# Kernel tuning notes

Measured on AMD Instinct MI355X. Metric: run time of the kernel, lower is better.

The kernel has to match this reference:

```python
import jax, jax.numpy as jnp
import numpy as np

N_ATOM_BASIS = 128
MAX_Z = 100
N_GAUSSIANS = 25
N_FILTERS = 128
R_CUTOFF = 5.0


def ssp(x):
    # shifted softplus: log(0.5*exp(x) + 0.5)
    return jax.nn.softplus(x) - jnp.log(2.0).astype(x.dtype)


def setup_inputs() -> dict:
    key = jax.random.key(0)
    ks = jax.random.split(key, 12)
    N, K = 20000, 48
    dR = jax.random.uniform(ks[0], (N, K), jnp.float32) * R_CUTOFF
    Z = jax.random.randint(ks[1], (N,), 0, MAX_Z, jnp.int32)
    neighbor_idx = jax.random.randint(ks[2], (N, K), 0, N + 1, jnp.int32)  # idx == N is padding
    s = 1.0 / np.sqrt(N_ATOM_BASIS)
    return {
        "dR": dR,
        "Z": Z,
        "neighbor_idx": neighbor_idx,
        "embed": jax.random.normal(ks[3], (MAX_Z, N_ATOM_BASIS), jnp.float32),
        "in2f_w": jax.random.normal(ks[4], (N_ATOM_BASIS, N_FILTERS), jnp.float32) * s,
        "f1_w": jax.random.normal(ks[5], (N_GAUSSIANS, N_FILTERS), jnp.float32) * (1.0 / np.sqrt(N_GAUSSIANS)),
        "f1_b": jnp.zeros((N_FILTERS,), jnp.float32),
        "f2_w": jax.random.normal(ks[6], (N_FILTERS, N_FILTERS), jnp.float32) * s,
        "f2_b": jnp.zeros((N_FILTERS,), jnp.float32),
        "o1_w": jax.random.normal(ks[7], (N_FILTERS, N_ATOM_BASIS), jnp.float32) * s,
        "o1_b": jnp.zeros((N_ATOM_BASIS,), jnp.float32),
        "o2_w": jax.random.normal(ks[8], (N_ATOM_BASIS, N_ATOM_BASIS), jnp.float32) * s,
        "o2_b": jnp.zeros((N_ATOM_BASIS,), jnp.float32),
    }


def reference(dR, Z, neighbor_idx, embed, in2f_w, f1_w, f1_b, f2_w, f2_b,
              o1_w, o1_b, o2_w, o2_b):
    N = Z.shape[0]
    # atom embedding [N, 128]
    x = embed[Z]

    # gaussian smearing of distances [N, K, 25]
    offsets = jnp.linspace(0.0, R_CUTOFF, N_GAUSSIANS, dtype=jnp.float32)
    width = offsets[1] - offsets[0]
    coeff = -0.5 / (width * width)
    g = jnp.exp(coeff * jnp.square(dR[..., None] - offsets))

    # filter-generating network [N, K, F]
    W = ssp(g @ f1_w + f1_b) @ f2_w + f2_b

    # cosine cutoff and pairwise (padding) mask
    cut = 0.5 * (jnp.cos(dR * (jnp.pi / R_CUTOFF)) + 1.0) * (dR < R_CUTOFF)
    mask = (neighbor_idx < N).astype(jnp.float32)  # [N, K]
    W = W * (cut * mask)[..., None]

    # continuous-filter convolution: project, gather neighbors, weight, aggregate
    y = x @ in2f_w                                  # [N, F]
    idx_safe = jnp.where(neighbor_idx < N, neighbor_idx, 0)
    y_nb = y[idx_safe]                              # [N, K, F] gather
    agg = jnp.sum(y_nb * W, axis=1)                 # [N, F]

    # output network + residual
    v = ssp(agg @ o1_w + o1_b) @ o2_w + o2_b
    return x + v
```

## Files before the change

kernel.cpp:

```cpp
#include <hip/hip_runtime.h>
#include <hip/hip_fp16.h>
#include <math.h>

constexpr int F    = 128;
constexpr int KN   = 48;
constexpr int NG   = 25;
constexpr int TN   = 176;
constexpr int MAXZ = 100;

typedef _Float16 f16x8 __attribute__((ext_vector_type(8)));
typedef float    f32x4 __attribute__((ext_vector_type(4)));

__device__ __forceinline__ float ssp(float x) {
    return fmaxf(x, 0.0f) + __logf(fmaf(0.5f, __expf(-fabsf(x)), 0.5f));
}

__device__ __forceinline__ unsigned short f2h(float x) {
    return __half_as_ushort(__float2half_rn(x));
}
__device__ __forceinline__ __half2 u2h2(unsigned int u) {
    union { unsigned int u; __half2 h; } c; c.u = u; return c.h;
}

__global__ __launch_bounds__(256) void k_prep(
    const float* __restrict__ f1w, const float* __restrict__ f1b,
    const float* __restrict__ f2w, const float* __restrict__ f2b,
    const float* __restrict__ o1w, const float* __restrict__ o2w,
    const float* __restrict__ embed, const float* __restrict__ in2f,
    unsigned int* __restrict__ tabp, unsigned int* __restrict__ yzp,
    unsigned short* __restrict__ o1f, unsigned short* __restrict__ o2f, int N)
{
    __shared__ float s0[F];
    __shared__ float s1[F];
    int bid = blockIdx.x;
    int tid = threadIdx.x;

    if (bid < TN + 1) {
        int j = bid, f = tid;
        float d = (float)j * (5.0f / (float)TN);
        constexpr float width = 5.0f / 24.0f;
        constexpr float coeff = -0.5f / (width * width);
        if (f < F) {
            float z = f1b[f];
            #pragma unroll
            for (int c = 0; c < NG; ++c) {
                float t = d - (float)c * width;
                z = fmaf(__expf(coeff * t * t), f1w[c * F + f], z);
            }
            s0[f] = ssp(z);
        }
        __syncthreads();
        if (f < F) {
            float w = f2b[f];
            #pragma unroll 8
            for (int c = 0; c < F; ++c)
                w = fmaf(s0[c], f2w[c * F + f], w);
            float cut = 0.5f * (cosf(d * 0.62831853071795864769f) + 1.0f);
            cut = (d < 5.0f) ? cut : 0.0f;
            s1[f] = w * cut;
        }
        __syncthreads();
        if (f < 64)
            tabp[j * 64 + f] = (unsigned int)f2h(s1[2 * f]) | ((unsigned int)f2h(s1[2 * f + 1]) << 16);
        return;
    }
    bid -= TN + 1;

    if (bid < 128) {
        int t = bid * 256 + tid;
        int e = t & 16383;
        int j = e & 7, l = (e >> 3) & 63, nt = (e >> 9) & 7, kt = e >> 12;
        int k = kt * 32 + ((l >> 4) << 3) + j;
        int col = nt * 16 + (l & 15);
        if (t < 16384) o1f[e] = f2h(o1w[k * F + col]);
        else           o2f[e] = f2h(o2w[k * F + col]);
        return;
    }
    bid -= 128;

    {
        int z = bid, f = tid;
        if (z < MAXZ) {
            if (f < F) s0[f] = embed[z * F + f];
            __syncthreads();
            if (f < F) {
                float acc = 0.f;
                #pragma unroll 8
                for (int c = 0; c < F; ++c)
                    acc = fmaf(s0[c], in2f[c * F + f], acc);
                s1[f] = acc;
            }
        } else {
            if (f < F) s1[f] = 0.f;
            __syncthreads();
        }
        __syncthreads();
        if (f < 64)
            yzp[z * 64 + f] = (unsigned int)f2h(s1[2 * f]) | ((unsigned int)f2h(s1[2 * f + 1]) << 16);
    }
}

__global__ __launch_bounds__(512, 6) void k_main(
    const float* __restrict__ dR, const int* __restrict__ nbr,
    const int* __restrict__ Z,
    const unsigned int* __restrict__ tabp,
    const unsigned int* __restrict__ yzp,
    const unsigned short* __restrict__ o1f, const float* __restrict__ o1b,
    const unsigned short* __restrict__ o2f, const float* __restrict__ o2b,
    const float* __restrict__ embed,
    float* __restrict__ out, int N, int ngroups)
{
    extern __shared__ unsigned int smem[];
    unsigned int*   tabL = smem;
    unsigned int*   aggL = smem + 11328;
    unsigned short* Us   = (unsigned short*)(smem + 11328 + 1024);

    int tid  = threadIdx.x;
    int wid  = tid >> 6;
    int lane = tid & 63;
    int lr   = lane & 15;
    int lg   = lane >> 4;

    for (int m = tid; m < (TN + 1) * 64; m += 512)
        tabL[m] = tabp[m];
    __syncthreads();

    for (int g = blockIdx.x; g < ngroups; g += gridDim.x) {
        int n0 = g * 16;

        int aA = wid * 2, aB = aA + 1;
        int nA = n0 + aA, nB = n0 + aB;
        float a0 = 0.f, a1 = 0.f, b0 = 0.f, b1 = 0.f;
        if (nA < N) {
            int mB = (nB < N) ? nB : nA;

            unsigned int pA = 0, pB = 0;
            if (lane < KN) {
                float dA = dR[nA * KN + lane];
                int   iA = nbr[nA * KN + lane];
                float uA = dA * ((float)TN / 5.0f);
                int   jA = (int)uA; jA = (jA > TN - 1) ? (TN - 1) : jA;
                float fA = uA - (float)jA;
                unsigned int zA = (iA >= 0 && iA < N) ? (unsigned int)Z[iA] : (unsigned int)MAXZ;
                pA = ((unsigned int)f2h(fA) << 16) | ((unsigned int)jA << 7) | zA;

                float dB = dR[mB * KN + lane];
                int   iB = nbr[mB * KN + lane];
                float uB = dB * ((float)TN / 5.0f);
                int   jB = (int)uB; jB = (jB > TN - 1) ? (TN - 1) : jB;
                float fB = uB - (float)jB;
                unsigned int zB = (iB >= 0 && iB < N) ? (unsigned int)Z[iB] : (unsigned int)MAXZ;
                pB = ((unsigned int)f2h(fB) << 16) | ((unsigned int)jB << 7) | zB;
            }

            #pragma unroll
            for (int c = 0; c < 4; ++c) {
                __half2 pacA = u2h2(0u);
                __half2 pacB = u2h2(0u);
                #pragma unroll
                for (int k2 = 0; k2 < 12; ++k2) {
                    int k = c * 12 + k2;
                    unsigned int qA = (unsigned int)__builtin_amdgcn_readlane((int)pA, k);
                    unsigned int qB = (unsigned int)__builtin_amdgcn_readlane((int)pB, k);

                    __half2 frA = u2h2((qA & 0xFFFF0000u) | (qA >> 16));
                    __half2 frB = u2h2((qB & 0xFFFF0000u) | (qB >> 16));
                    unsigned int jbA = (qA & 0x7F80u) << 1;
                    unsigned int jbB = (qB & 0x7F80u) << 1;
                    unsigned int zbA = (qA & 0x7Fu) << 8;
                    unsigned int zbB = (qB & 0x7Fu) << 8;

                    const unsigned int* rA = (const unsigned int*)((const char*)tabL + jbA);
                    const unsigned int* rB = (const unsigned int*)((const char*)tabL + jbB);
                    __half2 tA0 = u2h2(rA[lane]);
                    __half2 tA1 = u2h2(rA[lane + 64]);
                    __half2 tB0 = u2h2(rB[lane]);
                    __half2 tB1 = u2h2(rB[lane + 64]);
                    __half2 yA  = u2h2(*(const unsigned int*)((const char*)yzp + zbA + (lane << 2)));
                    __half2 yB  = u2h2(*(const unsigned int*)((const char*)yzp + zbB + (lane << 2)));

                    __half2 wA = __hfma2(frA, __hsub2(tA1, tA0), tA0);
                    __half2 wB = __hfma2(frB, __hsub2(tB1, tB0), tB0);
                    pacA = __hfma2(wA, yA, pacA);
                    pacB = __hfma2(wB, yB, pacB);
                }
                float2 fa = __half22float2(pacA); a0 += fa.x; a1 += fa.y;
                float2 fb = __half22float2(pacB); b0 += fb.x; b1 += fb.y;
            }
        }
        aggL[aA * 64 + (lane ^ (aA << 2))] = (unsigned int)f2h(a0) | ((unsigned int)f2h(a1) << 16);
        aggL[aB * 64 + (lane ^ (aB << 2))] = (unsigned int)f2h(b0) | ((unsigned int)f2h(b1) << 16);
        __syncthreads();

        f32x4 c1 = {0.f, 0.f, 0.f, 0.f};
        #pragma unroll
        for (int kt = 0; kt < 4; ++kt) {
            f16x8 b = *reinterpret_cast<const f16x8*>(o1f + (((kt * 8 + wid) * 64 + lane) << 3));
            const char* ap = (const char*)aggL + lr * 256 + ((kt * 64 + lg * 16) ^ (lr << 4));
            f16x8 a = *reinterpret_cast<const f16x8*>(ap);
            c1 = __builtin_amdgcn_mfma_f32_16x16x32_f16(a, b, c1, 0, 0, 0);
        }
        int fcol = wid * 16 + lr;
        float bv1 = o1b[fcol];
        #pragma unroll
        for (int jr = 0; jr < 4; ++jr) {
            int r = lg * 4 + jr;
            float u = ssp(c1[jr] + bv1);
            Us[r * F + (fcol ^ (r << 3))] = f2h(u);
        }
        __syncthreads();

        f32x4 c2 = {0.f, 0.f, 0.f, 0.f};
        #pragma unroll
        for (int kt = 0; kt < 4; ++kt) {
            f16x8 b = *reinterpret_cast<const f16x8*>(o2f + (((kt * 8 + wid) * 64 + lane) << 3));
            f16x8 a = *reinterpret_cast<const f16x8*>(&Us[lr * F + ((kt * 32 + lg * 8) ^ (lr << 3))]);
            c2 = __builtin_amdgcn_mfma_f32_16x16x32_f16(a, b, c2, 0, 0, 0);
        }
        float bv2 = o2b[fcol];
        #pragma unroll
        for (int jr = 0; jr < 4; ++jr) {
            int r = lg * 4 + jr;
            int n = n0 + r;
            if (n < N) {
                float x = embed[Z[n] * F + fcol];
                out[n * F + fcol] = x + c2[jr] + bv2;
            }
        }
    }
}

extern "C" void kernel_launch(void* const* d_in, const int* in_sizes, int n_in,
                              void* d_out, int out_size, void* d_ws, size_t ws_size,
                              hipStream_t stream) {
    const float* dR    = (const float*)d_in[0];
    const int*   Z     = (const int*)  d_in[1];
    const int*   nbr   = (const int*)  d_in[2];
    const float* embed = (const float*)d_in[3];
    const float* in2f  = (const float*)d_in[4];
    const float* f1w   = (const float*)d_in[5];
    const float* f1b   = (const float*)d_in[6];
    const float* f2w   = (const float*)d_in[7];
    const float* f2b   = (const float*)d_in[8];
    const float* o1w   = (const float*)d_in[9];
    const float* o1b   = (const float*)d_in[10];
    const float* o2w   = (const float*)d_in[11];
    const float* o2b   = (const float*)d_in[12];

    int N = in_sizes[1];

    char* wp = (char*)d_ws;
    unsigned int*   tabp = (unsigned int*)wp;   wp += (size_t)(TN + 1) * 64 * 4;
    unsigned int*   yzp  = (unsigned int*)wp;   wp += (size_t)(MAXZ + 1) * 64 * 4;
    unsigned short* o1f  = (unsigned short*)wp; wp += 16384 * 2;
    unsigned short* o2f  = (unsigned short*)wp;

    int grid_prep = (TN + 1) + 128 + (MAXZ + 1);

    int ngroups   = (N + 15) / 16;
    int grid_main = (ngroups < 768) ? ngroups : 768;
    int lds_main  = (TN + 1) * 64 * 4 + 4096 + 4096;

    (void)hipFuncSetAttribute((const void*)k_main,
                              hipFuncAttributeMaxDynamicSharedMemorySize, lds_main);

    k_prep<<<grid_prep, 256, 0, stream>>>(f1w, f1b, f2w, f2b, o1w, o2w,
                                          embed, in2f, tabp, yzp, o1f, o2f, N);
    k_main<<<grid_main, 512, lds_main, stream>>>(dR, nbr, Z, tabp, yzp,
                                                 o1f, o1b, o2f, o2b,
                                                 embed, (float*)d_out,
                                                 N, ngroups);
}
```

Before: 36.81 us.

## Replace LDS-interpolated filter table with dense global nearest-neighbor lookup table

The filter-network table grows from 177 rows with linear interpolation held in LDS to 4097 rows read directly from global memory (L2/L1) with nearest-row lookup. The prep kernel is restructured to compute 32 rows per block, staging the Gaussians in LDS. The per-pair work shrinks to one table load, one embedding load and one packed FMA, with no interpolation. With the LDS staging gone, occupancy hints rise (8 waves per SIMD, grid 1024), and a trailing barrier is added to the node loop. The cost is cached global reads for the 1 MB table in place of LDS reads, plus nearest-neighbor quantization error.

```diff
diff --git a/kernel.cpp b/kernel.cpp
--- a/kernel.cpp
+++ b/kernel.cpp
@@ -2,11 +2,11 @@
 #include <hip/hip_fp16.h>
 #include <math.h>
 
-constexpr int F    = 128;
-constexpr int KN   = 48;
-constexpr int NG   = 25;
-constexpr int TN   = 176;
-constexpr int MAXZ = 100;
+constexpr int F     = 128;
+constexpr int KN    = 48;
+constexpr int NG    = 25;
+constexpr int TROWS = 4096;
+constexpr int MAXZ  = 100;
 
 typedef _Float16 f16x8 __attribute__((ext_vector_type(8)));
 typedef float    f32x4 __attribute__((ext_vector_type(4)));
@@ -15,8 +15,8 @@
     return fmaxf(x, 0.0f) + __logf(fmaf(0.5f, __expf(-fabsf(x)), 0.5f));
 }
 
-__device__ __forceinline__ unsigned short f2h(float x) {
-    return __half_as_ushort(__float2half_rn(x));
+__device__ __forceinline__ unsigned int f2h(float x) {
+    return (unsigned int)__half_as_ushort(__float2half_rn(x));
 }
 __device__ __forceinline__ __half2 u2h2(unsigned int u) {
     union { unsigned int u; __half2 h; } c; c.u = u; return c.h;
@@ -27,44 +27,63 @@
     const float* __restrict__ f2w, const float* __restrict__ f2b,
     const float* __restrict__ o1w, const float* __restrict__ o2w,
     const float* __restrict__ embed, const float* __restrict__ in2f,
-    unsigned int* __restrict__ tabp, unsigned int* __restrict__ yzp,
+    unsigned int* __restrict__ tab6, unsigned int* __restrict__ yzp,
     unsigned short* __restrict__ o1f, unsigned short* __restrict__ o2f, int N)
 {
-    __shared__ float s0[F];
-    __shared__ float s1[F];
+    __shared__ float gsh[32][26];
+    __shared__ float hsh[32][F];
     int bid = blockIdx.x;
     int tid = threadIdx.x;
 
-    if (bid < TN + 1) {
-        int j = bid, f = tid;
-        float d = (float)j * (5.0f / (float)TN);
+    if (bid < 129) {
+        int r0 = bid * 32;
+        constexpr float hstep = 5.0f / (float)TROWS;
         constexpr float width = 5.0f / 24.0f;
         constexpr float coeff = -0.5f / (width * width);
-        if (f < F) {
-            float z = f1b[f];
-            #pragma unroll
-            for (int c = 0; c < NG; ++c) {
-                float t = d - (float)c * width;
-                z = fmaf(__expf(coeff * t * t), f1w[c * F + f], z);
-            }
-            s0[f] = ssp(z);
-        }
-        __syncthreads();
-        if (f < F) {
-            float w = f2b[f];
-            #pragma unroll 8
-            for (int c = 0; c < F; ++c)
-                w = fmaf(s0[c], f2w[c * F + f], w);
-            float cut = 0.5f * (cosf(d * 0.62831853071795864769f) + 1.0f);
-            cut = (d < 5.0f) ? cut : 0.0f;
-            s1[f] = w * cut;
-        }
-        __syncthreads();
-        if (f < 64)
-            tabp[j * 64 + f] = (unsigned int)f2h(s1[2 * f]) | ((unsigned int)f2h(s1[2 * f + 1]) << 16);
+
+        for (int e = tid; e < 32 * NG; e += 256) {
+            int rw = e / NG, c = e - rw * NG;
+            float d = (float)(r0 + rw) * hstep;
+            float t = d - (float)c * width;
+            gsh[rw][c] = __expf(coeff * t * t);
+        }
+        __syncthreads();
+        {
+            int f = tid & 127, rg = tid >> 7;
+            for (int i = 0; i < 16; ++i) {
+                int rw = i * 2 + rg;
+                float z = f1b[f];
+                #pragma unroll
+                for (int c = 0; c < NG; ++c)
+                    z = fmaf(gsh[rw][c], f1w[c * F + f], z);
+                hsh[rw][f] = ssp(z);
+            }
+        }
+        __syncthreads();
+        {
+            int l = tid & 63, rg = tid >> 6;
+            const float2 bv = *(const float2*)(f2b + 2 * l);
+            for (int i = 0; i < 8; ++i) {
+                int rw  = i * 4 + rg;
+                int row = r0 + rw;
+                if (row > TROWS) continue;
+                float w0 = bv.x, w1 = bv.y;
+                #pragma unroll 4
+                for (int c = 0; c < F; ++c) {
+                    float2 f2v = *(const float2*)(f2w + c * F + 2 * l);
+                    float  hv  = hsh[rw][c];
+                    w0 = fmaf(hv, f2v.x, w0);
+                    w1 = fmaf(hv, f2v.y, w1);
+                }
+                float d   = (float)row * hstep;
+                float cut = 0.5f * (cosf(d * 0.62831853071795864769f) + 1.0f);
+                cut = (d < 5.0f) ? cut : 0.0f;
+                tab6[row * 64 + l] = f2h(w0 * cut) | (f2h(w1 * cut) << 16);
+            }
+        }
         return;
     }
-    bid -= TN + 1;
+    bid -= 129;
 
     if (bid < 128) {
         int t = bid * 256 + tid;
@@ -72,14 +91,16 @@
         int j = e & 7, l = (e >> 3) & 63, nt = (e >> 9) & 7, kt = e >> 12;
         int k = kt * 32 + ((l >> 4) << 3) + j;
         int col = nt * 16 + (l & 15);
-        if (t < 16384) o1f[e] = f2h(o1w[k * F + col]);
-        else           o2f[e] = f2h(o2w[k * F + col]);
+        if (t < 16384) o1f[e] = (unsigned short)f2h(o1w[k * F + col]);
+        else           o2f[e] = (unsigned short)f2h(o2w[k * F + col]);
         return;
     }
     bid -= 128;
 
     {
         int z = bid, f = tid;
+        float* s0 = &hsh[0][0];
+        float* s1 = s0 + F;
         if (z < MAXZ) {
             if (f < F) s0[f] = embed[z * F + f];
             __syncthreads();
@@ -96,24 +117,22 @@
         }
         __syncthreads();
         if (f < 64)
-            yzp[z * 64 + f] = (unsigned int)f2h(s1[2 * f]) | ((unsigned int)f2h(s1[2 * f + 1]) << 16);
-    }
-}
-
-__global__ __launch_bounds__(512, 6) void k_main(
+            yzp[z * 64 + f] = f2h(s1[2 * f]) | (f2h(s1[2 * f + 1]) << 16);
+    }
+}
+
+__global__ __launch_bounds__(512, 8) void k_main(
     const float* __restrict__ dR, const int* __restrict__ nbr,
     const int* __restrict__ Z,
-    const unsigned int* __restrict__ tabp,
+    const unsigned int* __restrict__ tab6,
     const unsigned int* __restrict__ yzp,
     const unsigned short* __restrict__ o1f, const float* __restrict__ o1b,
     const unsigned short* __restrict__ o2f, const float* __restrict__ o2b,
     const float* __restrict__ embed,
     float* __restrict__ out, int N, int ngroups)
 {
-    extern __shared__ unsigned int smem[];
-    unsigned int*   tabL = smem;
-    unsigned int*   aggL = smem + 11328;
-    unsigned short* Us   = (unsigned short*)(smem + 11328 + 1024);
+    __shared__ unsigned int   aggL[1024];
+    __shared__ unsigned short Us[2048];
 
     int tid  = threadIdx.x;
     int wid  = tid >> 6;
@@ -121,10 +140,6 @@
     int lr   = lane & 15;
     int lg   = lane >> 4;
 
-    for (int m = tid; m < (TN + 1) * 64; m += 512)
-        tabL[m] = tabp[m];
-    __syncthreads();
-
     for (int g = blockIdx.x; g < ngroups; g += gridDim.x) {
         int n0 = g * 16;
 
@@ -138,20 +153,21 @@
             if (lane < KN) {
                 float dA = dR[nA * KN + lane];
                 int   iA = nbr[nA * KN + lane];
-                float uA = dA * ((float)TN / 5.0f);
-                int   jA = (int)uA; jA = (jA > TN - 1) ? (TN - 1) : jA;
-                float fA = uA - (float)jA;
+                int   jA = (int)(dA * ((float)TROWS / 5.0f) + 0.5f);
+                jA = (jA > TROWS) ? TROWS : jA;
                 unsigned int zA = (iA >= 0 && iA < N) ? (unsigned int)Z[iA] : (unsigned int)MAXZ;
-                pA = ((unsigned int)f2h(fA) << 16) | ((unsigned int)jA << 7) | zA;
+                pA = ((unsigned int)jA << 7) | zA;
 
                 float dB = dR[mB * KN + lane];
                 int   iB = nbr[mB * KN + lane];
-                float uB = dB * ((float)TN / 5.0f);
-                int   jB = (int)uB; jB = (jB > TN - 1) ? (TN - 1) : jB;
-                float fB = uB - (float)jB;
+                int   jB = (int)(dB * ((float)TROWS / 5.0f) + 0.5f);
+                jB = (jB > TROWS) ? TROWS : jB;
                 unsigned int zB = (iB >= 0 && iB < N) ? (unsigned int)Z[iB] : (unsigned int)MAXZ;
-                pB = ((unsigned int)f2h(fB) << 16) | ((unsigned int)jB << 7) | zB;
-            }
+                pB = ((unsigned int)jB << 7) | zB;
+            }
+
+            const char* tb = (const char*)tab6 + (lane << 2);
+            const char* yb = (const char*)yzp  + (lane << 2);
 
             #pragma unroll
             for (int c = 0; c < 4; ++c) {
@@ -163,33 +179,25 @@
                     unsigned int qA = (unsigned int)__builtin_amdgcn_readlane((int)pA, k);
                     unsigned int qB = (unsigned int)__builtin_amdgcn_readlane((int)pB, k);
 
-                    __half2 frA = u2h2((qA & 0xFFFF0000u) | (qA >> 16));
-                    __half2 frB = u2h2((qB & 0xFFFF0000u) | (qB >> 16));
-                    unsigned int jbA = (qA & 0x7F80u) << 1;
-                    unsigned int jbB = (qB & 0x7F80u) << 1;
+                    unsigned int jbA = (qA & 0xFFFFFF80u) << 1;
+                    unsigned int jbB = (qB & 0xFFFFFF80u) << 1;
                     unsigned int zbA = (qA & 0x7Fu) << 8;
                     unsigned int zbB = (qB & 0x7Fu) << 8;
 
-                    const unsigned int* rA = (const unsigned int*)((const char*)tabL + jbA);
-                    const unsigned int* rB = (const unsigned int*)((const char*)tabL + jbB);
-                    __half2 tA0 = u2h2(rA[lane]);
-                    __half2 tA1 = u2h2(rA[lane + 64]);
-                    __half2 tB0 = u2h2(rB[lane]);
-                    __half2 tB1 = u2h2(rB[lane + 64]);
-                    __half2 yA  = u2h2(*(const unsigned int*)((const char*)yzp + zbA + (lane << 2)));
-                    __half2 yB  = u2h2(*(const unsigned int*)((const char*)yzp + zbB + (lane << 2)));
-
-                    __half2 wA = __hfma2(frA, __hsub2(tA1, tA0), tA0);
-                    __half2 wB = __hfma2(frB, __hsub2(tB1, tB0), tB0);
-                    pacA = __hfma2(wA, yA, pacA);
-                    pacB = __hfma2(wB, yB, pacB);
+                    unsigned int tAv = *(const unsigned int*)(tb + jbA);
+                    unsigned int yAv = *(const unsigned int*)(yb + zbA);
+                    unsigned int tBv = *(const unsigned int*)(tb + jbB);
+                    unsigned int yBv = *(const unsigned int*)(yb + zbB);
+
+                    pacA = __hfma2(u2h2(tAv), u2h2(yAv), pacA);
+                    pacB = __hfma2(u2h2(tBv), u2h2(yBv), pacB);
                 }
                 float2 fa = __half22float2(pacA); a0 += fa.x; a1 += fa.y;
                 float2 fb = __half22float2(pacB); b0 += fb.x; b1 += fb.y;
             }
         }
-        aggL[aA * 64 + (lane ^ (aA << 2))] = (unsigned int)f2h(a0) | ((unsigned int)f2h(a1) << 16);
-        aggL[aB * 64 + (lane ^ (aB << 2))] = (unsigned int)f2h(b0) | ((unsigned int)f2h(b1) << 16);
+        aggL[aA * 64 + (lane ^ (aA << 2))] = f2h(a0) | (f2h(a1) << 16);
+        aggL[aB * 64 + (lane ^ (aB << 2))] = f2h(b0) | (f2h(b1) << 16);
         __syncthreads();
 
         f32x4 c1 = {0.f, 0.f, 0.f, 0.f};
@@ -206,7 +214,7 @@
         for (int jr = 0; jr < 4; ++jr) {
             int r = lg * 4 + jr;
             float u = ssp(c1[jr] + bv1);
-            Us[r * F + (fcol ^ (r << 3))] = f2h(u);
+            Us[r * F + (fcol ^ (r << 3))] = (unsigned short)f2h(u);
         }
         __syncthreads();
 
@@ -227,6 +235,7 @@
                 out[n * F + fcol] = x + c2[jr] + bv2;
             }
         }
+        __syncthreads();
     }
 }
 
@@ -250,24 +259,20 @@
     int N = in_sizes[1];
 
     char* wp = (char*)d_ws;
-    unsigned int*   tabp = (unsigned int*)wp;   wp += (size_t)(TN + 1) * 64 * 4;
+    unsigned int*   tab6 = (unsigned int*)wp;   wp += (size_t)(TROWS + 1) * 64 * 4;
     unsigned int*   yzp  = (unsigned int*)wp;   wp += (size_t)(MAXZ + 1) * 64 * 4;
     unsigned short* o1f  = (unsigned short*)wp; wp += 16384 * 2;
     unsigned short* o2f  = (unsigned short*)wp;
 
-    int grid_prep = (TN + 1) + 128 + (MAXZ + 1);
+    int grid_prep = 129 + 128 + (MAXZ + 1);
 
     int ngroups   = (N + 15) / 16;
-    int grid_main = (ngroups < 768) ? ngroups : 768;
-    int lds_main  = (TN + 1) * 64 * 4 + 4096 + 4096;
-
-    (void)hipFuncSetAttribute((const void*)k_main,
-                              hipFuncAttributeMaxDynamicSharedMemorySize, lds_main);
+    int grid_main = (ngroups < 1024) ? ngroups : 1024;
 
     k_prep<<<grid_prep, 256, 0, stream>>>(f1w, f1b, f2w, f2b, o1w, o2w,
-                                          embed, in2f, tabp, yzp, o1f, o2f, N);
-    k_main<<<grid_main, 512, lds_main, stream>>>(dR, nbr, Z, tabp, yzp,
-                                                 o1f, o1b, o2f, o2b,
-                                                 embed, (float*)d_out,
-                                                 N, ngroups);
-}
+                                          embed, in2f, tab6, yzp, o1f, o2f, N);
+    k_main<<<grid_main, 512, 0, stream>>>(dR, nbr, Z, tab6, yzp,
+                                          o1f, o1b, o2f, o2b,
+                                          embed, (float*)d_out,
+                                          N, ngroups);
+}
```

Result: slower. 86.51 us (+135.0%).
